# Kernel optimization log

Hardware: AMD Instinct MI355X
Metric: run time of the kernel (lower is better)

The kernel has to match this reference:

```python
import jax, jax.numpy as jnp
import numpy as np

NUM_FILTERS = 10


def _peaking(cos_w0, alpha, A):
    aA = alpha * A
    aiA = alpha / A
    Bs = jnp.stack([1 + aA, -2 * cos_w0, 1 - aA], axis=-1)
    As = jnp.stack([1 + aiA, -2 * cos_w0, 1 - aiA], axis=-1)
    return Bs, As


def _low_shelf(cos_w0, alpha, A):
    Ap1, Am1 = A + 1, A - 1
    tsa = 2 * jnp.sqrt(A) * alpha
    Bs = jnp.stack([A * (Ap1 - Am1 * cos_w0 + tsa),
                    2 * A * (Am1 - Ap1 * cos_w0),
                    A * (Ap1 - Am1 * cos_w0 - tsa)], axis=-1)
    As = jnp.stack([Ap1 + Am1 * cos_w0 + tsa,
                    -2 * (Am1 + Ap1 * cos_w0),
                    Ap1 + Am1 * cos_w0 - tsa], axis=-1)
    return Bs, As


def _high_shelf(cos_w0, alpha, A):
    Ap1, Am1 = A + 1, A - 1
    tsa = 2 * jnp.sqrt(A) * alpha
    Bs = jnp.stack([A * (Ap1 + Am1 * cos_w0 + tsa),
                    -2 * A * (Am1 + Ap1 * cos_w0),
                    A * (Ap1 + Am1 * cos_w0 - tsa)], axis=-1)
    As = jnp.stack([Ap1 - Am1 * cos_w0 + tsa,
                    2 * (Am1 - Ap1 * cos_w0),
                    Ap1 - Am1 * cos_w0 - tsa], axis=-1)
    return Bs, As


def _coefficients(w0, q_inv, log_gain):
    # Parameter activations (BaseParametricEqualizerFilter)
    w0 = jnp.pi * jax.nn.sigmoid(w0)
    q_inv = jnp.exp(q_inv)
    A = jnp.exp(log_gain)
    cos_w0 = jnp.cos(w0)
    alpha = jnp.sin(w0) * q_inv * 0.5
    K = w0.shape[-1]
    # split [1, K-2, 1]: low-shelf | peaking | high-shelf
    Bs_ls, As_ls = _low_shelf(cos_w0[..., :1], alpha[..., :1], A[..., :1])
    Bs_pk, As_pk = _peaking(cos_w0[..., 1:K - 1], alpha[..., 1:K - 1], A[..., 1:K - 1])
    Bs_hs, As_hs = _high_shelf(cos_w0[..., K - 1:], alpha[..., K - 1:], A[..., K - 1:])
    Bs = jnp.concatenate([Bs_ls, Bs_pk, Bs_hs], axis=-2)  # (B, C, K, 3)
    As = jnp.concatenate([As_ls, As_pk, As_hs], axis=-2)
    return Bs, As


def _cascade_biquad(x, Bs, As):
    # x: (B, C, L); Bs/As: (B, C, K, 3). Exact cascaded biquad, DF2-transposed.
    b = Bs / As[..., :1]
    a = As / As[..., :1]
    b0, b1, b2 = (jnp.moveaxis(b[..., i], -1, 0) for i in range(3))  # each (K, B, C)
    a1, a2 = (jnp.moveaxis(a[..., i], -1, 0) for i in (1, 2))
    K = b0.shape[0]
    xt = jnp.moveaxis(x, -1, 0)  # (L, B, C)
    s0 = jnp.zeros((K,) + x.shape[:-1], x.dtype)

    def step(carry, x_t):
        s1, s2 = carry  # (K, B, C)
        y = x_t
        ns1, ns2 = [], []
        for k in range(K):  # fixed small cascade, unrolled
            xk = y
            y = b0[k] * xk + s1[k]
            ns1.append(b1[k] * xk - a1[k] * y + s2[k])
            ns2.append(b2[k] * xk - a2[k] * y)
        return (jnp.stack(ns1), jnp.stack(ns2)), y

    _, yt = jax.lax.scan(step, (s0, s0), xt)
    return jnp.moveaxis(yt, 0, -1)  # (B, C, L)


def setup_inputs() -> dict:
    key = jax.random.key(0)
    k1, k2, k3, k4 = jax.random.split(key, 4)
    B, C, L, K = 256, 1, 65536, NUM_FILTERS
    return {
        "input_signals": jax.random.normal(k1, (B, C, L), jnp.float32),
        "w0": jax.random.normal(k2, (B, C, K), jnp.float32),
        "q_inv": jax.random.normal(k3, (B, C, K), jnp.float32),
        "log_gain": jax.random.normal(k4, (B, C, K), jnp.float32) * 0.3,
    }


def reference(input_signals, w0, q_inv, log_gain):
    Bs, As = _coefficients(w0, q_inv, log_gain)
    return _cascade_biquad(input_signals, Bs, As)
```

## Files before the change

kernel.cpp:

```cpp
#include <hip/hip_runtime.h>
#include <math.h>

#ifndef M_PI
#define M_PI 3.14159265358979323846
#endif

#define NFILT   10
#define THREADS 1024
#define CHUNK   32
#define HALF    32768
#define LTOT    65536
#define NWAVE   (THREADS / 64)

#define WS_STRIDE 576
#define MATS_OFF  96

typedef float v2f __attribute__((ext_vector_type(2)));
__device__ inline v2f mk2(float a, float b) { v2f r; r.x = a; r.y = b; return r; }
__device__ inline v2f fs(float s) { return mk2(s, s); }
#define F2(a,b,c) __builtin_elementwise_fma((a),(b),(c))


__device__ inline void biquad_coefs(int k, double w0r, double qir, double gr,
                                    double* bo, double* ao) {
    const double w0 = M_PI / (1.0 + exp(-w0r));
    const double qi = exp(qir);
    const double A  = exp(gr);
    const double cw = cos(w0);
    const double al = sin(w0) * qi * 0.5;
    double B0, B1, B2, A0, A1, A2;
    if (k == 0) {
        const double Ap1 = A + 1.0, Am1 = A - 1.0, tsa = 2.0 * sqrt(A) * al;
        B0 = A * (Ap1 - Am1 * cw + tsa);
        B1 = 2.0 * A * (Am1 - Ap1 * cw);
        B2 = A * (Ap1 - Am1 * cw - tsa);
        A0 = Ap1 + Am1 * cw + tsa;
        A1 = -2.0 * (Am1 + Ap1 * cw);
        A2 = Ap1 + Am1 * cw - tsa;
    } else if (k == NFILT - 1) {
        const double Ap1 = A + 1.0, Am1 = A - 1.0, tsa = 2.0 * sqrt(A) * al;
        B0 = A * (Ap1 + Am1 * cw + tsa);
        B1 = -2.0 * A * (Am1 + Ap1 * cw);
        B2 = A * (Ap1 + Am1 * cw - tsa);
        A0 = Ap1 - Am1 * cw + tsa;
        A1 = 2.0 * (Am1 - Ap1 * cw);
        A2 = Ap1 - Am1 * cw - tsa;
    } else {
        const double aA = al * A, aiA = al / A;
        B0 = 1.0 + aA;  B1 = -2.0 * cw; B2 = 1.0 - aA;
        A0 = 1.0 + aiA; A1 = B1;        A2 = 1.0 - aiA;
    }
    const double inv = 1.0 / A0;
    bo[0] = B0 * inv; bo[1] = B1 * inv; bo[2] = B2 * inv;
    ao[0] = 1.0;      ao[1] = A1 * inv; ao[2] = A2 * inv;
}

__global__ void eq_precompute_kernel(const float* __restrict__ w0_in,
                                     const float* __restrict__ qinv_in,
                                     const float* __restrict__ gain_in,
                                     float* __restrict__ ws)
{
    const int b = blockIdx.x;
    const int j = threadIdx.x;
    if (j >= NFILT) return;

    double bo[3], ao[3];
    biquad_coefs(j, (double)w0_in[b*NFILT+j], (double)qinv_in[b*NFILT+j],
                 (double)gain_in[b*NFILT+j], bo, ao);

    float* wb = ws + (size_t)b * WS_STRIDE;
    float* cj = wb + j * 8;
    cj[0] = (float)bo[0]; cj[1] = (float)bo[1]; cj[2] = (float)bo[2];
    cj[3] = (float)ao[1]; cj[4] = (float)ao[2];

    double m0 = -ao[1], m1 = -ao[2], m2 = 1.0, m3 = 0.0;
    #pragma unroll
    for (int i = 0; i < 5; ++i) {
        const double n0 = m0*m0 + m1*m2, n1 = m0*m1 + m1*m3;
        const double n2 = m2*m0 + m3*m2, n3 = m2*m1 + m3*m3;
        m0 = n0; m1 = n1; m2 = n2; m3 = n3;
    }
    for (int r = 0; r < 10; ++r) {
        float* mr = wb + MATS_OFF + j*40 + r*4;
        mr[0] = (float)m0; mr[1] = (float)m1; mr[2] = (float)m2; mr[3] = (float)m3;
        const double n0 = m0*m0 + m1*m2, n1 = m0*m1 + m1*m3;
        const double n2 = m2*m0 + m3*m2, n3 = m2*m1 + m3*m3;
        m0 = n0; m1 = n1; m2 = n2; m3 = n3;
    }
}


__global__ void
__attribute__((amdgpu_flat_work_group_size(THREADS, THREADS)))
__attribute__((amdgpu_waves_per_eu(4, 4)))
eq_cascade_kernel(const float* __restrict__ x,
                  float* __restrict__ out,
                  const float* __restrict__ ws)
{
    __shared__ float4 sigh[8][THREADS];
    __shared__ float4 bndA[THREADS];
    __shared__ float4 waveP[2][NWAVE];

    const int tid  = threadIdx.x;
    const int lane = tid & 63;
    const int wid  = tid >> 6;
    const int b    = blockIdx.x;
    const float* __restrict__ wsb = ws + (size_t)b * WS_STRIDE;

    const float* xb = x   + (size_t)b * LTOT;
    float*       ob = out + (size_t)b * LTOT;

    v2f sig[16];

    const float4* s0 = reinterpret_cast<const float4*>(xb + (size_t)tid * CHUNK);
    const float4* s1 = reinterpret_cast<const float4*>(xb + HALF + (size_t)tid * CHUNK);
    #pragma unroll
    for (int i = 0; i < 4; ++i) {
        const float4 a = s0[i], c = s1[i];
        sig[4*i+0] = mk2(a.x, c.x); sig[4*i+1] = mk2(a.y, c.y);
        sig[4*i+2] = mk2(a.z, c.z); sig[4*i+3] = mk2(a.w, c.w);
    }
    float4 la, lc;
    #pragma unroll
    for (int i = 0; i < 4; ++i) {
        const float4 a = s0[4+i], c = s1[4+i];
        sigh[2*i][tid]   = make_float4(a.x, c.x, a.y, c.y);
        sigh[2*i+1][tid] = make_float4(a.z, c.z, a.w, c.w);
        if (i == 3) { la = a; lc = c; }
    }
    bndA[tid] = make_float4(la.w, la.z, lc.w, lc.z);
    __syncthreads();

    v2f xw1, xw2;
    if (tid == 0) {
        const float4 t = bndA[THREADS-1];
        xw1 = mk2(0.f, t.x); xw2 = mk2(0.f, t.y);
    } else {
        const float4 t = bndA[tid-1];
        xw1 = mk2(t.x, t.z); xw2 = mk2(t.y, t.w);
    }

    v2f i1 = mk2(0.f,0.f), i2 = mk2(0.f,0.f);
    float pa1 = 0.f, pa2 = 0.f;

    #pragma unroll 1
    for (int j = 0; j < NFILT; ++j) {
        const float* cj = wsb + j*8;
        const float b0 = cj[0], b1c = cj[1], b2 = cj[2], a1 = cj[3], a2 = cj[4];
        const float* mb = wsb + MATS_OFF + j*40;
        const v2f nb0 = fs(b0), nb1 = fs(b1c), nb2 = fs(b2);
        const v2f na1 = fs(-a1), na2 = fs(-a2);
        const v2f np1 = fs(-pa1), np2 = fs(-pa2);

        v2f u1, u2, z1 = mk2(0.f,0.f), z2 = mk2(0.f,0.f);
        if (j == 0) { u1 = xw1; u2 = xw2; } else { u1 = i1; u2 = i2; }

        if (j == 0) {
            #pragma unroll
            for (int t = 0; t < 16; ++t) {
                const v2f u = sig[t];
                const v2f c = F2(nb0, u, F2(nb1, u1, nb2*u2));
                const v2f z = F2(na1, z1, F2(na2, z2, c));
                sig[t] = c; u2 = u1; u1 = u; z2 = z1; z1 = z;
            }
            #pragma unroll
            for (int i = 0; i < 8; ++i) {
                const float4 v = sigh[i][tid];
                v2f p = mk2(v.x, v.y), q = mk2(v.z, v.w);
                {
                    const v2f u = p;
                    const v2f c = F2(nb0, u, F2(nb1, u1, nb2*u2));
                    const v2f z = F2(na1, z1, F2(na2, z2, c));
                    p = c; u2 = u1; u1 = u; z2 = z1; z1 = z;
                }
                {
                    const v2f u = q;
                    const v2f c = F2(nb0, u, F2(nb1, u1, nb2*u2));
                    const v2f z = F2(na1, z1, F2(na2, z2, c));
                    q = c; u2 = u1; u1 = u; z2 = z1; z1 = z;
                }
                sigh[i][tid] = make_float4(p.x, p.y, q.x, q.y);
            }
        } else {
            #pragma unroll
            for (int t = 0; t < 16; ++t) {
                const v2f u = F2(np1, u1, F2(np2, u2, sig[t]));
                const v2f c = F2(nb0, u, F2(nb1, u1, nb2*u2));
                const v2f z = F2(na1, z1, F2(na2, z2, c));
                sig[t] = c; u2 = u1; u1 = u; z2 = z1; z1 = z;
            }
            #pragma unroll
            for (int i = 0; i < 8; ++i) {
                const float4 v = sigh[i][tid];
                v2f p = mk2(v.x, v.y), q = mk2(v.z, v.w);
                {
                    const v2f u = F2(np1, u1, F2(np2, u2, p));
                    const v2f c = F2(nb0, u, F2(nb1, u1, nb2*u2));
                    const v2f z = F2(na1, z1, F2(na2, z2, c));
                    p = c; u2 = u1; u1 = u; z2 = z1; z1 = z;
                }
                {
                    const v2f u = F2(np1, u1, F2(np2, u2, q));
                    const v2f c = F2(nb0, u, F2(nb1, u1, nb2*u2));
                    const v2f z = F2(na1, z1, F2(na2, z2, c));
                    q = c; u2 = u1; u1 = u; z2 = z1; z1 = z;
                }
                sigh[i][tid] = make_float4(p.x, p.y, q.x, q.y);
            }
        }

        v2f Sa = z1, Sb = z2;
        #pragma unroll
        for (int r = 0; r < 6; ++r) {
            const int d = 1 << r;
            const float4 M = *reinterpret_cast<const float4*>(mb + r*4);
            float tax = __shfl_up(Sa.x, d, 64), tay = __shfl_up(Sa.y, d, 64);
            float tbx = __shfl_up(Sb.x, d, 64), tby = __shfl_up(Sb.y, d, 64);
            const bool act = (lane >= d);
            tax = act ? tax : 0.f; tay = act ? tay : 0.f;
            tbx = act ? tbx : 0.f; tby = act ? tby : 0.f;
            const v2f ta = mk2(tax, tay), tb = mk2(tbx, tby);
            Sa = F2(fs(M.x), ta, F2(fs(M.y), tb, Sa));
            Sb = F2(fs(M.z), ta, F2(fs(M.w), tb, Sb));
        }
        const int buf = j & 1;
        if (lane == 63) waveP[buf][wid] = make_float4(Sa.x, Sa.y, Sb.x, Sb.y);
        __syncthreads();

        const float4 Pv = waveP[buf][lane & 15];
        v2f Ta = mk2(Pv.x, Pv.y), Tb = mk2(Pv.z, Pv.w);
        #pragma unroll
        for (int l = 0; l < 4; ++l) {
            const int d = 1 << l;
            const float4 M = *reinterpret_cast<const float4*>(mb + (6+l)*4);
            float tax = __shfl_up(Ta.x, d, 64), tay = __shfl_up(Ta.y, d, 64);
            float tbx = __shfl_up(Tb.x, d, 64), tby = __shfl_up(Tb.y, d, 64);
            const bool act = (lane >= d);
            tax = act ? tax : 0.f; tay = act ? tay : 0.f;
            tbx = act ? tbx : 0.f; tby = act ? tby : 0.f;
            const v2f ta = mk2(tax, tay), tb = mk2(tbx, tby);
            Ta = F2(fs(M.x), ta, F2(fs(M.y), tb, Ta));
            Tb = F2(fs(M.z), ta, F2(fs(M.w), tb, Tb));
        }

        const float h0a = __shfl(Ta.x, 15, 64);
        const float h0b = __shfl(Tb.x, 15, 64);
        float vax = __shfl(Ta.x, wid - 1, 64), vay = __shfl(Ta.y, wid - 1, 64);
        float vbx = __shfl(Tb.x, wid - 1, 64), vby = __shfl(Tb.y, wid - 1, 64);
        if (wid == 0) { vax = vay = vbx = vby = 0.f; }
        {
            float hx = h0a, hy = h0b;
            #pragma unroll
            for (int l = 0; l < 4; ++l) {
                const float4 M = *reinterpret_cast<const float4*>(mb + (6+l)*4);
                const bool bit = (wid >> l) & 1;
                const float nx = M.x * hx + M.y * hy;
                const float ny = M.z * hx + M.w * hy;
                hx = bit ? nx : hx; hy = bit ? ny : hy;
            }
            vay += hx; vby += hy;
        }
        v2f Va = mk2(vax, vay), Vb = mk2(vbx, vby);
        #pragma unroll
        for (int r = 0; r < 6; ++r) {
            const float4 M = *reinterpret_cast<const float4*>(mb + r*4);
            const bool bit = (lane >> r) & 1;
            const v2f Na = F2(fs(M.x), Va, fs(M.y) * Vb);
            const v2f Nb = F2(fs(M.z), Va, fs(M.w) * Vb);
            Va = bit ? Na : Va;
            Vb = bit ? Nb : Vb;
        }
        {
            float eax = __shfl_up(Sa.x, 1, 64), eay = __shfl_up(Sa.y, 1, 64);
            float ebx = __shfl_up(Sb.x, 1, 64), eby = __shfl_up(Sb.y, 1, 64);
            if (lane == 0) { eax = eay = ebx = eby = 0.f; }
            i1 = Va + mk2(eax, eay);
            i2 = Vb + mk2(ebx, eby);
        }
        pa1 = a1; pa2 = a2;
    }

    {
        v2f u1 = i1, u2 = i2;
        const v2f np1 = fs(-pa1), np2 = fs(-pa2);
        float4* d0 = reinterpret_cast<float4*>(ob + (size_t)tid * CHUNK);
        float4* d1 = reinterpret_cast<float4*>(ob + HALF + (size_t)tid * CHUNK);
        #pragma unroll
        for (int i = 0; i < 4; ++i) {
            float4 a, c;
            #pragma unroll
            for (int e = 0; e < 4; ++e) {
                const v2f u = F2(np1, u1, F2(np2, u2, sig[4*i+e]));
                (&a.x)[e] = u.x; (&c.x)[e] = u.y;
                u2 = u1; u1 = u;
            }
            d0[i] = a; d1[i] = c;
        }
        #pragma unroll
        for (int i = 0; i < 4; ++i) {
            const float4 v = sigh[2*i][tid], w = sigh[2*i+1][tid];
            const v2f s0v = mk2(v.x, v.y), s1v = mk2(v.z, v.w);
            const v2f s2v = mk2(w.x, w.y), s3v = mk2(w.z, w.w);
            float4 a, c;
            v2f u;
            u = F2(np1, u1, F2(np2, u2, s0v)); a.x = u.x; c.x = u.y; u2 = u1; u1 = u;
            u = F2(np1, u1, F2(np2, u2, s1v)); a.y = u.x; c.y = u.y; u2 = u1; u1 = u;
            u = F2(np1, u1, F2(np2, u2, s2v)); a.z = u.x; c.z = u.y; u2 = u1; u1 = u;
            u = F2(np1, u1, F2(np2, u2, s3v)); a.w = u.x; c.w = u.y; u2 = u1; u1 = u;
            d0[4+i] = a; d1[4+i] = c;
        }
    }
}

extern "C" void kernel_launch(void* const* d_in, const int* in_sizes, int n_in,
                              void* d_out, int out_size, void* d_ws, size_t ws_size,
                              hipStream_t stream) {
    const float* x    = (const float*)d_in[0];
    const float* w0   = (const float*)d_in[1];
    const float* qinv = (const float*)d_in[2];
    const float* gain = (const float*)d_in[3];
    float* out = (float*)d_out;
    float* ws  = (float*)d_ws;

    const int B = in_sizes[1] / NFILT;
    eq_precompute_kernel<<<B, 64, 0, stream>>>(w0, qinv, gain, ws);
    eq_cascade_kernel<<<B, THREADS, 0, stream>>>(x, out, ws);
}
```

Before: 88.37 us.

## Split each thread's chunk into two contiguous halves and shrink scan to scalar

Each thread now owns a contiguous 64-sample chunk instead of two 32-sample slices separated by half the signal. The two halves are processed as the v2f lanes and then composed using the chunk-length transition matrix (M32). This lets the inter-thread and inter-wave prefix scans carry one scalar state pair instead of a two-lane vector, which removes the per-half fixup step, halves the shuffle and LDS traffic, and shrinks the boundary and wave buffers. It adds a small 2x2 matrix apply before and after the scan, and global loads become one contiguous 256-byte run per thread.

```diff
diff --git a/kernel.cpp b/kernel.cpp
--- a/kernel.cpp
+++ b/kernel.cpp
@@ -7,9 +7,8 @@
 
 #define NFILT   10
 #define THREADS 1024
-#define CHUNK   32
-#define HALF    32768
-#define LTOT    65536
+#define CHUNK   64
+#define LTOT    (THREADS * CHUNK)
 #define NWAVE   (THREADS / 64)
 
 #define WS_STRIDE 576
@@ -80,8 +79,17 @@
         const double n2 = m2*m0 + m3*m2, n3 = m2*m1 + m3*m3;
         m0 = n0; m1 = n1; m2 = n2; m3 = n3;
     }
+    {
+        float* mr = wb + MATS_OFF + j*44 + 10*4;
+        mr[0] = (float)m0; mr[1] = (float)m1; mr[2] = (float)m2; mr[3] = (float)m3;
+    }
+    {
+        const double n0 = m0*m0 + m1*m2, n1 = m0*m1 + m1*m3;
+        const double n2 = m2*m0 + m3*m2, n3 = m2*m1 + m3*m3;
+        m0 = n0; m1 = n1; m2 = n2; m3 = n3;
+    }
     for (int r = 0; r < 10; ++r) {
-        float* mr = wb + MATS_OFF + j*40 + r*4;
+        float* mr = wb + MATS_OFF + j*44 + r*4;
         mr[0] = (float)m0; mr[1] = (float)m1; mr[2] = (float)m2; mr[3] = (float)m3;
         const double n0 = m0*m0 + m1*m2, n1 = m0*m1 + m1*m3;
         const double n2 = m2*m0 + m3*m2, n3 = m2*m1 + m3*m3;
@@ -98,8 +106,8 @@
                   const float* __restrict__ ws)
 {
     __shared__ float4 sigh[8][THREADS];
-    __shared__ float4 bndA[THREADS];
-    __shared__ float4 waveP[2][NWAVE];
+    __shared__ float2 bnd[THREADS];
+    __shared__ float2 waveP[2][NWAVE];
 
     const int tid  = threadIdx.x;
     const int lane = tid & 63;
@@ -112,32 +120,37 @@
 
     v2f sig[16];
 
-    const float4* s0 = reinterpret_cast<const float4*>(xb + (size_t)tid * CHUNK);
-    const float4* s1 = reinterpret_cast<const float4*>(xb + HALF + (size_t)tid * CHUNK);
+    const float4* src = reinterpret_cast<const float4*>(xb + (size_t)tid * CHUNK);
+    float4 fx[8];
+    #pragma unroll
+    for (int i = 0; i < 8; ++i) fx[i] = src[i];
+    float4 fy[8];
+    #pragma unroll
+    for (int i = 0; i < 8; ++i) fy[i] = src[8 + i];
+
     #pragma unroll
     for (int i = 0; i < 4; ++i) {
-        const float4 a = s0[i], c = s1[i];
-        sig[4*i+0] = mk2(a.x, c.x); sig[4*i+1] = mk2(a.y, c.y);
-        sig[4*i+2] = mk2(a.z, c.z); sig[4*i+3] = mk2(a.w, c.w);
-    }
-    float4 la, lc;
+        sig[4*i+0] = mk2((&fx[i].x)[0], (&fy[i].x)[0]);
+        sig[4*i+1] = mk2((&fx[i].x)[1], (&fy[i].x)[1]);
+        sig[4*i+2] = mk2((&fx[i].x)[2], (&fy[i].x)[2]);
+        sig[4*i+3] = mk2((&fx[i].x)[3], (&fy[i].x)[3]);
+    }
     #pragma unroll
     for (int i = 0; i < 4; ++i) {
-        const float4 a = s0[4+i], c = s1[4+i];
+        const float4 a = fx[4+i], c = fy[4+i];
         sigh[2*i][tid]   = make_float4(a.x, c.x, a.y, c.y);
         sigh[2*i+1][tid] = make_float4(a.z, c.z, a.w, c.w);
-        if (i == 3) { la = a; lc = c; }
-    }
-    bndA[tid] = make_float4(la.w, la.z, lc.w, lc.z);
+    }
+    const float xty1 = fx[7].w, xty2 = fx[7].z;
+    bnd[tid] = make_float2(fy[7].w, fy[7].z);
     __syncthreads();
 
     v2f xw1, xw2;
-    if (tid == 0) {
-        const float4 t = bndA[THREADS-1];
-        xw1 = mk2(0.f, t.x); xw2 = mk2(0.f, t.y);
-    } else {
-        const float4 t = bndA[tid-1];
-        xw1 = mk2(t.x, t.z); xw2 = mk2(t.y, t.w);
+    {
+        float h1 = 0.f, h2 = 0.f;
+        if (tid > 0) { const float2 t = bnd[tid-1]; h1 = t.x; h2 = t.y; }
+        xw1 = mk2(h1, xty1);
+        xw2 = mk2(h2, xty2);
     }
 
     v2f i1 = mk2(0.f,0.f), i2 = mk2(0.f,0.f);
@@ -147,7 +160,7 @@
     for (int j = 0; j < NFILT; ++j) {
         const float* cj = wsb + j*8;
         const float b0 = cj[0], b1c = cj[1], b2 = cj[2], a1 = cj[3], a2 = cj[4];
-        const float* mb = wsb + MATS_OFF + j*40;
+        const float* mb = wsb + MATS_OFF + j*44;
         const v2f nb0 = fs(b0), nb1 = fs(b1c), nb2 = fs(b2);
         const v2f na1 = fs(-a1), na2 = fs(-a2);
         const v2f np1 = fs(-pa1), np2 = fs(-pa2);
@@ -209,74 +222,64 @@
             }
         }
 
-        v2f Sa = z1, Sb = z2;
+        const float4 M32 = *reinterpret_cast<const float4*>(mb + 10*4);
+        float Sa = M32.x * z1.x + M32.y * z2.x + z1.y;
+        float Sb = M32.z * z1.x + M32.w * z2.x + z2.y;
+
         #pragma unroll
         for (int r = 0; r < 6; ++r) {
             const int d = 1 << r;
             const float4 M = *reinterpret_cast<const float4*>(mb + r*4);
-            float tax = __shfl_up(Sa.x, d, 64), tay = __shfl_up(Sa.y, d, 64);
-            float tbx = __shfl_up(Sb.x, d, 64), tby = __shfl_up(Sb.y, d, 64);
+            float ta = __shfl_up(Sa, d, 64);
+            float tb = __shfl_up(Sb, d, 64);
             const bool act = (lane >= d);
-            tax = act ? tax : 0.f; tay = act ? tay : 0.f;
-            tbx = act ? tbx : 0.f; tby = act ? tby : 0.f;
-            const v2f ta = mk2(tax, tay), tb = mk2(tbx, tby);
-            Sa = F2(fs(M.x), ta, F2(fs(M.y), tb, Sa));
-            Sb = F2(fs(M.z), ta, F2(fs(M.w), tb, Sb));
+            ta = act ? ta : 0.f;
+            tb = act ? tb : 0.f;
+            Sa = Sa + M.x * ta + M.y * tb;
+            Sb = Sb + M.z * ta + M.w * tb;
         }
         const int buf = j & 1;
-        if (lane == 63) waveP[buf][wid] = make_float4(Sa.x, Sa.y, Sb.x, Sb.y);
+        if (lane == 63) waveP[buf][wid] = make_float2(Sa, Sb);
         __syncthreads();
 
-        const float4 Pv = waveP[buf][lane & 15];
-        v2f Ta = mk2(Pv.x, Pv.y), Tb = mk2(Pv.z, Pv.w);
+        const float2 Pv = waveP[buf][lane & 15];
+        float Tx = Pv.x, Ty = Pv.y;
         #pragma unroll
         for (int l = 0; l < 4; ++l) {
             const int d = 1 << l;
             const float4 M = *reinterpret_cast<const float4*>(mb + (6+l)*4);
-            float tax = __shfl_up(Ta.x, d, 64), tay = __shfl_up(Ta.y, d, 64);
-            float tbx = __shfl_up(Tb.x, d, 64), tby = __shfl_up(Tb.y, d, 64);
+            float tx = __shfl_up(Tx, d, 64);
+            float ty = __shfl_up(Ty, d, 64);
             const bool act = (lane >= d);
-            tax = act ? tax : 0.f; tay = act ? tay : 0.f;
-            tbx = act ? tbx : 0.f; tby = act ? tby : 0.f;
-            const v2f ta = mk2(tax, tay), tb = mk2(tbx, tby);
-            Ta = F2(fs(M.x), ta, F2(fs(M.y), tb, Ta));
-            Tb = F2(fs(M.z), ta, F2(fs(M.w), tb, Tb));
-        }
-
-        const float h0a = __shfl(Ta.x, 15, 64);
-        const float h0b = __shfl(Tb.x, 15, 64);
-        float vax = __shfl(Ta.x, wid - 1, 64), vay = __shfl(Ta.y, wid - 1, 64);
-        float vbx = __shfl(Tb.x, wid - 1, 64), vby = __shfl(Tb.y, wid - 1, 64);
-        if (wid == 0) { vax = vay = vbx = vby = 0.f; }
-        {
-            float hx = h0a, hy = h0b;
-            #pragma unroll
-            for (int l = 0; l < 4; ++l) {
-                const float4 M = *reinterpret_cast<const float4*>(mb + (6+l)*4);
-                const bool bit = (wid >> l) & 1;
-                const float nx = M.x * hx + M.y * hy;
-                const float ny = M.z * hx + M.w * hy;
-                hx = bit ? nx : hx; hy = bit ? ny : hy;
-            }
-            vay += hx; vby += hy;
-        }
-        v2f Va = mk2(vax, vay), Vb = mk2(vbx, vby);
+            tx = act ? tx : 0.f;
+            ty = act ? ty : 0.f;
+            Tx = Tx + M.x * tx + M.y * ty;
+            Ty = Ty + M.z * tx + M.w * ty;
+        }
+        float Vx = __shfl(Tx, wid - 1, 64);
+        float Vy = __shfl(Ty, wid - 1, 64);
+        if (wid == 0) { Vx = 0.f; Vy = 0.f; }
         #pragma unroll
         for (int r = 0; r < 6; ++r) {
             const float4 M = *reinterpret_cast<const float4*>(mb + r*4);
             const bool bit = (lane >> r) & 1;
-            const v2f Na = F2(fs(M.x), Va, fs(M.y) * Vb);
-            const v2f Nb = F2(fs(M.z), Va, fs(M.w) * Vb);
-            Va = bit ? Na : Va;
-            Vb = bit ? Nb : Vb;
+            const float nx = M.x * Vx + M.y * Vy;
+            const float ny = M.z * Vx + M.w * Vy;
+            Vx = bit ? nx : Vx;
+            Vy = bit ? ny : Vy;
         }
         {
-            float eax = __shfl_up(Sa.x, 1, 64), eay = __shfl_up(Sa.y, 1, 64);
-            float ebx = __shfl_up(Sb.x, 1, 64), eby = __shfl_up(Sb.y, 1, 64);
-            if (lane == 0) { eax = eay = ebx = eby = 0.f; }
-            i1 = Va + mk2(eax, eay);
-            i2 = Vb + mk2(ebx, eby);
-        }
+            float Ea = __shfl_up(Sa, 1, 64);
+            float Eb = __shfl_up(Sb, 1, 64);
+            const bool l0 = (lane == 0);
+            Vx += l0 ? 0.f : Ea;
+            Vy += l0 ? 0.f : Eb;
+        }
+
+        const float iy1 = M32.x * Vx + M32.y * Vy + z1.x;
+        const float iy2 = M32.z * Vx + M32.w * Vy + z2.x;
+        i1 = mk2(Vx, iy1);
+        i2 = mk2(Vy, iy2);
         pa1 = a1; pa2 = a2;
     }
 
@@ -284,7 +287,7 @@
         v2f u1 = i1, u2 = i2;
         const v2f np1 = fs(-pa1), np2 = fs(-pa2);
         float4* d0 = reinterpret_cast<float4*>(ob + (size_t)tid * CHUNK);
-        float4* d1 = reinterpret_cast<float4*>(ob + HALF + (size_t)tid * CHUNK);
+        float4* d1 = reinterpret_cast<float4*>(ob + (size_t)tid * CHUNK + 32);
         #pragma unroll
         for (int i = 0; i < 4; ++i) {
             float4 a, c;
```

New measurement: 76.15 us. 13.8% less time.
